# Performance work log

Measured on AMD Instinct MI355X. Metric: run time of the kernel, lower is better.

## Reference

```python
import jax, jax.numpy as jnp
import numpy as np

B, S, DIM = 4, 2048, 1024


def _xavier(key, shape):
    # xavier_uniform for a [out, in] Linear weight
    fan_in, fan_out = shape[1], shape[0]
    limit = float(np.sqrt(6.0 / (fan_in + fan_out)))
    return jax.random.uniform(key, shape, jnp.float32, -limit, limit)


def setup_inputs() -> dict:
    key = jax.random.key(0)
    ks = jax.random.split(key, 8)
    z_real = jax.random.normal(ks[0], (B, S, DIM), jnp.float32)
    z_imag = jax.random.normal(ks[1], (B, S, DIM), jnp.float32)
    wq_r = _xavier(ks[2], (DIM, DIM))
    wq_i = _xavier(ks[3], (DIM, DIM))
    wk_r = _xavier(ks[4], (DIM, DIM))
    wk_i = _xavier(ks[5], (DIM, DIM))
    wv_r = _xavier(ks[6], (DIM, DIM))
    wv_i = _xavier(ks[7], (DIM, DIM))
    # causal mask (0 = masked), broadcast over batch
    mask = jnp.tril(jnp.ones((S, S), jnp.int32))
    return {"z_real": z_real, "z_imag": z_imag,
            "wq_r": wq_r, "wq_i": wq_i,
            "wk_r": wk_r, "wk_i": wk_i,
            "wv_r": wv_r, "wv_i": wv_i,
            "mask": mask}


def _complex_linear(xr, xi, wr, wi):
    # torch Linear: y = x @ W^T
    yr = xr @ wr.T - xi @ wi.T
    yi = xi @ wr.T + xr @ wi.T
    return yr, yi


def reference(z_real, z_imag, wq_r, wq_i, wk_r, wk_i, wv_r, wv_i, mask):
    dim = z_real.shape[-1]
    scale = dim ** (-0.5)
    qr, qi = _complex_linear(z_real, z_imag, wq_r, wq_i)
    kr, ki = _complex_linear(z_real, z_imag, wk_r, wk_i)
    vr, vi = _complex_linear(z_real, z_imag, wv_r, wv_i)
    # cat([q.real, q.imag]) @ cat([k.real, k.imag])^T == qr@kr^T + qi@ki^T
    scores = (jnp.einsum('bsd,btd->bst', qr, kr)
              + jnp.einsum('bsd,btd->bst', qi, ki)) * scale  # [B,S,S]
    scores = jnp.where(mask == 0, -jnp.inf, scores)
    attn = jax.nn.softmax(scores, axis=-1)
    out_r = jnp.einsum('bst,btd->bsd', attn, vr)
    out_i = jnp.einsum('bst,btd->bsd', attn, vi)
    return jnp.stack([out_r, out_i], axis=0)  # [2,B,S,dim] = (real, imag)
```

## Files before the change

kernel.cpp:

```cpp
#include <hip/hip_runtime.h>
#include <hip/hip_bf16.h>
#include <hip/hip_fp16.h>

#define DIMK 1024
#define SEQ  2048
#define BATCH 4
#define NTOK (BATCH*SEQ)
#define PROJ_ELEMS ((size_t)NTOK*DIMK)
#define LD 2048

typedef unsigned short ushort_t;
typedef __attribute__((ext_vector_type(8))) short short8;
typedef __attribute__((ext_vector_type(4))) float float4v;

#define MFMA_BF16 __builtin_amdgcn_mfma_f32_16x16x32_bf16

__device__ __forceinline__ unsigned short f2bf(float f) {
    union { float f; unsigned int i; } x; x.f = f;
    unsigned int r = x.i + 0x7fffu + ((x.i >> 16) & 1u);
    return (unsigned short)(r >> 16);
}

__device__ __forceinline__ void gld_lds16(const void* g, void* l) {
    auto gp = reinterpret_cast<const __attribute__((address_space(1))) unsigned int*>(
        reinterpret_cast<uintptr_t>(g));
    auto lp = reinterpret_cast<__attribute__((address_space(3))) unsigned int*>(
        reinterpret_cast<uintptr_t>(l));
    __builtin_amdgcn_global_load_lds(gp, lp, 16, 0, 0);
}

__device__ __forceinline__ void stage2(const ushort_t* __restrict__ gbase,
                                       ushort_t* lbase, int kcol,
                                       int rg0, int g, int scol)
{
    gld_lds16(gbase + (size_t)(rg0 * 16 + g) * LD + kcol + scol,
              lbase + rg0 * 512);
    gld_lds16(gbase + (size_t)(rg0 * 16 + 16 + g) * LD + kcol + scol,
              lbase + rg0 * 512 + 512);
}

__device__ __forceinline__ void gemm_core256(
    const ushort_t* __restrict__ Arow,
    const ushort_t* __restrict__ Brow,
    int kend,
    ushort_t* Alds, ushort_t* Blds,
    float4v acc[8][4], int wid, int lane)
{
    const int g    = lane >> 2;
    const int sx   = lane & 3;
    const int scol = ((sx - (g >> 1)) & 3) * 8;
    const int r16  = lane & 15;
    const int quad = lane >> 4;
    const int roff = r16 * 32 + ((quad + (r16 >> 1)) & 3) * 8;
    const int wm8 = (wid >> 2) * 8;
    const int wn4 = (wid & 3) * 4;
    const int rg0 = wid * 2;
    const int NT = kend >> 6;

    short8 a0[4], b0[4], a1[4], b1[4];

    stage2(Brow, Blds,        0,  rg0, g, scol);
    stage2(Arow, Alds,        0,  rg0, g, scol);
    stage2(Brow, Blds + 8192, 32, rg0, g, scol);
    stage2(Arow, Alds + 8192, 32, rg0, g, scol);
    asm volatile("s_waitcnt vmcnt(4)" ::: "memory");
    __builtin_amdgcn_s_barrier();
    #pragma unroll
    for (int j = 0; j < 4; ++j)
        b0[j] = *(const short8*)(Blds + (wn4 + j) * 512 + roff);
    #pragma unroll
    for (int i = 0; i < 4; ++i)
        a0[i] = *(const short8*)(Alds + (wm8 + i) * 512 + roff);

    for (int t = 0; t < NT; ++t) {
        const int d     = (t & 1) << 14;
        const int dn    = d ^ 16384;
        const int knext = (t + 1) << 6;
        const bool pre  = (t + 1 < NT);

        #pragma unroll
        for (int j = 0; j < 4; ++j)
            b1[j] = *(const short8*)(Blds + d + (wn4 + j) * 512 + roff);
        #pragma unroll
        for (int i = 0; i < 4; ++i)
            a1[i] = *(const short8*)(Alds + d + (wm8 + 4 + i) * 512 + roff);
        if (pre) {
            stage2(Brow, Blds + dn, knext, rg0, g, scol);
            stage2(Arow, Alds + dn, knext, rg0, g, scol);
        }
        asm volatile("" ::: "memory");
        __builtin_amdgcn_s_barrier();
        __builtin_amdgcn_s_setprio(1);
        #pragma unroll
        for (int i = 0; i < 4; ++i)
            #pragma unroll
            for (int j = 0; j < 4; ++j)
                acc[i][j] = MFMA_BF16(a0[i], b0[j], acc[i][j], 0, 0, 0);
        __builtin_amdgcn_s_setprio(0);
        if (pre) asm volatile("s_waitcnt vmcnt(4)" ::: "memory");
        else     asm volatile("s_waitcnt vmcnt(0)" ::: "memory");
        __builtin_amdgcn_s_barrier();

        #pragma unroll
        for (int j = 0; j < 4; ++j)
            b0[j] = *(const short8*)(Blds + d + 8192 + (wn4 + j) * 512 + roff);
        #pragma unroll
        for (int i = 0; i < 4; ++i)
            a0[i] = *(const short8*)(Alds + d + 8192 + (wm8 + i) * 512 + roff);
        if (pre) {
            stage2(Brow, Blds + dn + 8192, knext + 32, rg0, g, scol);
            stage2(Arow, Alds + dn + 8192, knext + 32, rg0, g, scol);
        }
        asm volatile("" ::: "memory");
        __builtin_amdgcn_s_barrier();
        __builtin_amdgcn_s_setprio(1);
        #pragma unroll
        for (int i = 0; i < 4; ++i)
            #pragma unroll
            for (int j = 0; j < 4; ++j)
                acc[4 + i][j] = MFMA_BF16(a1[i], b1[j], acc[4 + i][j], 0, 0, 0);
        __builtin_amdgcn_s_setprio(0);
        asm volatile("" ::: "memory");
        __builtin_amdgcn_s_barrier();

        #pragma unroll
        for (int j = 0; j < 4; ++j)
            b1[j] = *(const short8*)(Blds + d + 8192 + (wn4 + j) * 512 + roff);
        #pragma unroll
        for (int i = 0; i < 4; ++i)
            a1[i] = *(const short8*)(Alds + d + 8192 + (wm8 + 4 + i) * 512 + roff);
        asm volatile("" ::: "memory");
        __builtin_amdgcn_s_barrier();
        __builtin_amdgcn_s_setprio(1);
        #pragma unroll
        for (int i = 0; i < 4; ++i)
            #pragma unroll
            for (int j = 0; j < 4; ++j)
                acc[i][j] = MFMA_BF16(a0[i], b0[j], acc[i][j], 0, 0, 0);
        __builtin_amdgcn_s_setprio(0);
        if (pre) asm volatile("s_waitcnt vmcnt(4)" ::: "memory");
        __builtin_amdgcn_s_barrier();

        if (pre) {
            #pragma unroll
            for (int j = 0; j < 4; ++j)
                b0[j] = *(const short8*)(Blds + dn + (wn4 + j) * 512 + roff);
            #pragma unroll
            for (int i = 0; i < 4; ++i)
                a0[i] = *(const short8*)(Alds + dn + (wm8 + i) * 512 + roff);
        }
        asm volatile("" ::: "memory");
        __builtin_amdgcn_s_barrier();
        __builtin_amdgcn_s_setprio(1);
        #pragma unroll
        for (int i = 0; i < 4; ++i)
            #pragma unroll
            for (int j = 0; j < 4; ++j)
                acc[4 + i][j] = MFMA_BF16(a1[i], b1[j], acc[4 + i][j], 0, 0, 0);
        __builtin_amdgcn_s_setprio(0);
        asm volatile("" ::: "memory");
        __builtin_amdgcn_s_barrier();
    }
}

__global__ __launch_bounds__(512, 2)
void gemm_proj(const ushort_t* __restrict__ A, const ushort_t* __restrict__ B,
               ushort_t* __restrict__ Cq, ushort_t* __restrict__ Ck,
               ushort_t* __restrict__ Cv)
{
    __shared__ ushort_t smem[65536];
    const int tid = threadIdx.x, wid = tid >> 6, lane = tid & 63;
    const int m0 = blockIdx.y * 256;
    const int n0g = blockIdx.x * 256;
    ushort_t* C = (n0g < 2048) ? Cq : ((n0g < 4096) ? Ck : Cv);
    const int n0 = n0g & 2047;
    float4v acc[8][4] = {};
    gemm_core256(A + (size_t)m0 * LD, B + (size_t)n0g * LD, 2048,
                 smem, smem + 32768, acc, wid, lane);

    const int wm = wid >> 2, wn = wid & 3;
    const int col16 = lane & 15, quad = lane >> 4;
    #pragma unroll
    for (int i = 0; i < 8; ++i)
        #pragma unroll
        for (int j = 0; j < 4; ++j) {
            const int n = n0 + wn * 64 + j * 16 + col16;
            #pragma unroll
            for (int r = 0; r < 4; ++r) {
                const int m = m0 + wm * 128 + i * 16 + quad * 4 + r;
                C[(size_t)m * LD + n] = f2bf(acc[i][j][r]);
            }
        }
}

__global__ __launch_bounds__(512, 2)
void gemm_scores(const ushort_t* __restrict__ Q, const ushort_t* __restrict__ K,
                 __half* __restrict__ S)
{
    const int jt = blockIdx.x, it = blockIdx.y, b = blockIdx.z;
    if (jt > it) return;
    __shared__ ushort_t smem[65536];
    const int tid = threadIdx.x, wid = tid >> 6, lane = tid & 63;
    const size_t boff = (size_t)b * SEQ * LD;
    float4v acc[8][4] = {};
    gemm_core256(Q + boff + (size_t)it * 256 * LD, K + boff + (size_t)jt * 256 * LD,
                 2048, smem, smem + 32768, acc, wid, lane);

    const int wm = wid >> 2, wn = wid & 3;
    const int col16 = lane & 15, quad = lane >> 4;
    const float scale = 0.03125f;
    __half* Sb = S + (size_t)b * SEQ * SEQ;
    #pragma unroll
    for (int i = 0; i < 8; ++i)
        #pragma unroll
        for (int j = 0; j < 4; ++j) {
            const int t = jt * 256 + wn * 64 + j * 16 + col16;
            #pragma unroll
            for (int r = 0; r < 4; ++r) {
                const int s = it * 256 + wm * 128 + i * 16 + quad * 4 + r;
                Sb[(size_t)s * SEQ + t] = __float2half(acc[i][j][r] * scale);
            }
        }
}

__global__ __launch_bounds__(512, 2)
void gemm_pv(const ushort_t* __restrict__ P, const ushort_t* __restrict__ VT,
             float* __restrict__ out)
{
    const int nt = blockIdx.x, mt = blockIdx.y, b = blockIdx.z;
    __shared__ ushort_t smem[65536];
    const int tid = threadIdx.x, wid = tid >> 6, lane = tid & 63;
    const int kend = (mt + 1) * 256;
    float4v acc[8][4] = {};
    gemm_core256(P + (size_t)b * SEQ * SEQ + (size_t)mt * 256 * LD,
                 VT + (size_t)b * LD * LD + (size_t)nt * 256 * LD,
                 kend, smem, smem + 32768, acc, wid, lane);

    const int wm = wid >> 2, wn = wid & 3;
    const int col16 = lane & 15, quad = lane >> 4;
    #pragma unroll
    for (int i = 0; i < 8; ++i)
        #pragma unroll
        for (int j = 0; j < 4; ++j) {
            const int n = nt * 256 + wn * 64 + j * 16 + col16;
            float* dst = out + ((n < 1024) ? 0 : PROJ_ELEMS);
            const int d = n & 1023;
            #pragma unroll
            for (int r = 0; r < 4; ++r) {
                const int s = mt * 256 + wm * 128 + i * 16 + quad * 4 + r;
                dst[((size_t)b * SEQ + s) * DIMK + d] = acc[i][j][r];
            }
        }
}

__global__ __launch_bounds__(256)
void zcat_kernel(const float* __restrict__ zr, const float* __restrict__ zi,
                 ushort_t* __restrict__ zcat)
{
    const size_t e = ((size_t)blockIdx.x * 256 + threadIdx.x) * 8;
    const size_t tok = e >> 11;
    const int c = (int)(e & 2047);
    const float* src = (c < 1024) ? (zr + tok * 1024 + c) : (zi + tok * 1024 + (c - 1024));
    float4 a = *(const float4*)src;
    float4 b = *(const float4*)(src + 4);
    ushort_t* d = zcat + e;
    d[0]=f2bf(a.x); d[1]=f2bf(a.y); d[2]=f2bf(a.z); d[3]=f2bf(a.w);
    d[4]=f2bf(b.x); d[5]=f2bf(b.y); d[6]=f2bf(b.z); d[7]=f2bf(b.w);
}

__global__ __launch_bounds__(256)
void wstack_kernel(const float* __restrict__ wr, const float* __restrict__ wi,
                   ushort_t* __restrict__ ws)
{
    const size_t e = ((size_t)blockIdx.x * 256 + threadIdx.x) * 8;
    const int n = (int)(e >> 11), c = (int)(e & 2047);
    const int n1 = n & 1023, c1 = c & 1023;
    const float* src;
    float sgn = 1.f;
    if (n < 1024) {
        if (c < 1024) src = wr + (size_t)n1 * 1024 + c1;
        else        { src = wi + (size_t)n1 * 1024 + c1; sgn = -1.f; }
    } else {
        src = ((c < 1024) ? wi : wr) + (size_t)n1 * 1024 + c1;
    }
    float4 a = *(const float4*)src;
    float4 b = *(const float4*)(src + 4);
    ushort_t* d = ws + e;
    d[0]=f2bf(sgn*a.x); d[1]=f2bf(sgn*a.y); d[2]=f2bf(sgn*a.z); d[3]=f2bf(sgn*a.w);
    d[4]=f2bf(sgn*b.x); d[5]=f2bf(sgn*b.y); d[6]=f2bf(sgn*b.z); d[7]=f2bf(sgn*b.w);
}

__global__ __launch_bounds__(256)
void transpose_v(const ushort_t* __restrict__ vcat, ushort_t* __restrict__ vt)
{
    __shared__ ushort_t tile[64][65];
    const int b = blockIdx.z;
    const int t0 = blockIdx.x * 64, c0 = blockIdx.y * 64;
    const int tid = threadIdx.x;
    const int r = tid >> 4, c4 = (tid & 15) * 4;
    const ushort_t* src = vcat + ((size_t)(b * SEQ + t0)) * LD + c0;
    #pragma unroll
    for (int p = 0; p < 4; ++p) {
        const int row = p * 16 + r;
        ushort4 v = *(const ushort4*)(src + (size_t)row * LD + c4);
        tile[row][c4+0]=v.x; tile[row][c4+1]=v.y; tile[row][c4+2]=v.z; tile[row][c4+3]=v.w;
    }
    __syncthreads();
    ushort_t* dst = vt + ((size_t)b * LD + c0) * LD + t0;
    #pragma unroll
    for (int p = 0; p < 4; ++p) {
        const int crow = p * 16 + r;
        ushort4 v;
        v.x = tile[c4+0][crow]; v.y = tile[c4+1][crow];
        v.z = tile[c4+2][crow]; v.w = tile[c4+3][crow];
        *(ushort4*)(dst + (size_t)crow * LD + c4) = v;
    }
}

__global__ __launch_bounds__(256)
void softmax_kernel(__half* __restrict__ sc)
{
    const int row = blockIdx.x;
    const int s = row & (SEQ - 1);
    __half* x = sc + (size_t)row * SEQ;
    ushort_t* xo = (ushort_t*)x;
    const int n = s + 1;
    const int tid = threadIdx.x, wave = tid >> 6, lane = tid & 63;
    __shared__ float redm[4], reds[4];

    float m = -1e30f;
    for (int i = tid; i < n; i += 256) m = fmaxf(m, __half2float(x[i]));
    #pragma unroll
    for (int off = 32; off > 0; off >>= 1) m = fmaxf(m, __shfl_down(m, off, 64));
    if (lane == 0) redm[wave] = m;
    __syncthreads();
    if (tid == 0) redm[0] = fmaxf(fmaxf(redm[0], redm[1]), fmaxf(redm[2], redm[3]));
    __syncthreads();
    m = redm[0];

    float l = 0.f;
    for (int i = tid; i < n; i += 256) l += __expf(__half2float(x[i]) - m);
    #pragma unroll
    for (int off = 32; off > 0; off >>= 1) l += __shfl_down(l, off, 64);
    if (lane == 0) reds[wave] = l;
    __syncthreads();
    if (tid == 0) reds[0] = reds[0] + reds[1] + reds[2] + reds[3];
    __syncthreads();
    const float inv = 1.0f / reds[0];

    const int npad = min(SEQ, ((s >> 8) + 1) << 8);
    for (int i = tid; i < npad; i += 256) {
        float v = (i < n) ? __expf(__half2float(x[i]) - m) * inv : 0.f;
        xo[i] = f2bf(v);
    }
}

extern "C" void kernel_launch(void* const* d_in, const int* in_sizes, int n_in,
                              void* d_out, int out_size, void* d_ws, size_t ws_size,
                              hipStream_t stream)
{
    const float* z_real = (const float*)d_in[0];
    const float* z_imag = (const float*)d_in[1];
    const float* wq_r   = (const float*)d_in[2];
    const float* wq_i   = (const float*)d_in[3];
    const float* wk_r   = (const float*)d_in[4];
    const float* wk_i   = (const float*)d_in[5];
    const float* wv_r   = (const float*)d_in[6];
    const float* wv_i   = (const float*)d_in[7];

    uint8_t* ws = (uint8_t*)d_ws;
    ushort_t* zcat = (ushort_t*)(ws + 0);
    ushort_t* wall = (ushort_t*)(ws + 33554432);
    ushort_t* wsq  = wall;
    ushort_t* wsk  = (ushort_t*)(ws + 33554432 + 8388608);
    ushort_t* wsv  = (ushort_t*)(ws + 33554432 + 16777216);
    ushort_t* qcat = (ushort_t*)(ws + 58720256);
    ushort_t* kcat = (ushort_t*)(ws + 92274688);
    ushort_t* vcat = (ushort_t*)(ws + 125829120);
    ushort_t* vt   = (ushort_t*)(ws + 0);
    __half*   sc   = (__half*)(ws + 125829120);
    float*    outp = (float*)d_out;

    zcat_kernel<<<dim3(8192), dim3(256), 0, stream>>>(z_real, z_imag, zcat);
    wstack_kernel<<<dim3(2048), dim3(256), 0, stream>>>(wq_r, wq_i, wsq);
    wstack_kernel<<<dim3(2048), dim3(256), 0, stream>>>(wk_r, wk_i, wsk);
    wstack_kernel<<<dim3(2048), dim3(256), 0, stream>>>(wv_r, wv_i, wsv);

    gemm_proj<<<dim3(24, 32), dim3(512), 0, stream>>>(zcat, wall, qcat, kcat, vcat);

    transpose_v<<<dim3(32, 32, 4), dim3(256), 0, stream>>>(vcat, vt);
    gemm_scores<<<dim3(8, 8, 4), dim3(512), 0, stream>>>(qcat, kcat, sc);
    softmax_kernel<<<dim3(NTOK), dim3(256), 0, stream>>>(sc);
    gemm_pv<<<dim3(8, 8, 4), dim3(512), 0, stream>>>((ushort_t*)sc, vt, outp);
}
```

Baseline: 518.9 us.

## Simplify GEMM main loop to two barrier phases per k-tile

Restructures the projection GEMM inner loop. Register double-buffering of A/B fragments across half-steps is dropped: each half-tile now loads all A and B fragments from LDS and issues all 32 MFMAs at once. This cuts the barriers per 64-wide k-tile from eight to two, to reduce synchronisation overhead. The cost is less overlap between LDS reads and MFMA inside a wave, so latency hiding now depends more on other resident waves.

Measured after the change: 473.0 us. 1.1x faster.

```diff
diff --git a/kernel.cpp b/kernel.cpp
--- a/kernel.cpp
+++ b/kernel.cpp
@@ -57,45 +57,44 @@
     const int rg0 = wid * 2;
     const int NT = kend >> 6;
 
-    short8 a0[4], b0[4], a1[4], b1[4];
-
     stage2(Brow, Blds,        0,  rg0, g, scol);
     stage2(Arow, Alds,        0,  rg0, g, scol);
     stage2(Brow, Blds + 8192, 32, rg0, g, scol);
     stage2(Arow, Alds + 8192, 32, rg0, g, scol);
     asm volatile("s_waitcnt vmcnt(4)" ::: "memory");
     __builtin_amdgcn_s_barrier();
-    #pragma unroll
-    for (int j = 0; j < 4; ++j)
-        b0[j] = *(const short8*)(Blds + (wn4 + j) * 512 + roff);
-    #pragma unroll
-    for (int i = 0; i < 4; ++i)
-        a0[i] = *(const short8*)(Alds + (wm8 + i) * 512 + roff);
 
     for (int t = 0; t < NT; ++t) {
         const int d     = (t & 1) << 14;
         const int dn    = d ^ 16384;
         const int knext = (t + 1) << 6;
         const bool pre  = (t + 1 < NT);
+        short8 af0[4], af1[4], bf[4];
 
         #pragma unroll
         for (int j = 0; j < 4; ++j)
-            b1[j] = *(const short8*)(Blds + d + (wn4 + j) * 512 + roff);
-        #pragma unroll
-        for (int i = 0; i < 4; ++i)
-            a1[i] = *(const short8*)(Alds + d + (wm8 + 4 + i) * 512 + roff);
+            bf[j] = *(const short8*)(Blds + d + (wn4 + j) * 512 + roff);
+        #pragma unroll
+        for (int i = 0; i < 4; ++i)
+            af0[i] = *(const short8*)(Alds + d + (wm8 + i) * 512 + roff);
+        #pragma unroll
+        for (int i = 0; i < 4; ++i)
+            af1[i] = *(const short8*)(Alds + d + (wm8 + 4 + i) * 512 + roff);
         if (pre) {
             stage2(Brow, Blds + dn, knext, rg0, g, scol);
             stage2(Arow, Alds + dn, knext, rg0, g, scol);
         }
-        asm volatile("" ::: "memory");
-        __builtin_amdgcn_s_barrier();
         __builtin_amdgcn_s_setprio(1);
         #pragma unroll
         for (int i = 0; i < 4; ++i)
             #pragma unroll
             for (int j = 0; j < 4; ++j)
-                acc[i][j] = MFMA_BF16(a0[i], b0[j], acc[i][j], 0, 0, 0);
+                acc[i][j] = MFMA_BF16(af0[i], bf[j], acc[i][j], 0, 0, 0);
+        #pragma unroll
+        for (int i = 0; i < 4; ++i)
+            #pragma unroll
+            for (int j = 0; j < 4; ++j)
+                acc[4 + i][j] = MFMA_BF16(af1[i], bf[j], acc[4 + i][j], 0, 0, 0);
         __builtin_amdgcn_s_setprio(0);
         if (pre) asm volatile("s_waitcnt vmcnt(4)" ::: "memory");
         else     asm volatile("s_waitcnt vmcnt(0)" ::: "memory");
@@ -103,62 +102,30 @@
 
         #pragma unroll
         for (int j = 0; j < 4; ++j)
-            b0[j] = *(const short8*)(Blds + d + 8192 + (wn4 + j) * 512 + roff);
-        #pragma unroll
-        for (int i = 0; i < 4; ++i)
-            a0[i] = *(const short8*)(Alds + d + 8192 + (wm8 + i) * 512 + roff);
+            bf[j] = *(const short8*)(Blds + d + 8192 + (wn4 + j) * 512 + roff);
+        #pragma unroll
+        for (int i = 0; i < 4; ++i)
+            af0[i] = *(const short8*)(Alds + d + 8192 + (wm8 + i) * 512 + roff);
+        #pragma unroll
+        for (int i = 0; i < 4; ++i)
+            af1[i] = *(const short8*)(Alds + d + 8192 + (wm8 + 4 + i) * 512 + roff);
         if (pre) {
             stage2(Brow, Blds + dn + 8192, knext + 32, rg0, g, scol);
             stage2(Arow, Alds + dn + 8192, knext + 32, rg0, g, scol);
         }
-        asm volatile("" ::: "memory");
-        __builtin_amdgcn_s_barrier();
         __builtin_amdgcn_s_setprio(1);
         #pragma unroll
         for (int i = 0; i < 4; ++i)
             #pragma unroll
             for (int j = 0; j < 4; ++j)
-                acc[4 + i][j] = MFMA_BF16(a1[i], b1[j], acc[4 + i][j], 0, 0, 0);
-        __builtin_amdgcn_s_setprio(0);
-        asm volatile("" ::: "memory");
-        __builtin_amdgcn_s_barrier();
-
-        #pragma unroll
-        for (int j = 0; j < 4; ++j)
-            b1[j] = *(const short8*)(Blds + d + 8192 + (wn4 + j) * 512 + roff);
-        #pragma unroll
-        for (int i = 0; i < 4; ++i)
-            a1[i] = *(const short8*)(Alds + d + 8192 + (wm8 + 4 + i) * 512 + roff);
-        asm volatile("" ::: "memory");
-        __builtin_amdgcn_s_barrier();
-        __builtin_amdgcn_s_setprio(1);
+                acc[i][j] = MFMA_BF16(af0[i], bf[j], acc[i][j], 0, 0, 0);
         #pragma unroll
         for (int i = 0; i < 4; ++i)
             #pragma unroll
             for (int j = 0; j < 4; ++j)
-                acc[i][j] = MFMA_BF16(a0[i], b0[j], acc[i][j], 0, 0, 0);
+                acc[4 + i][j] = MFMA_BF16(af1[i], bf[j], acc[4 + i][j], 0, 0, 0);
         __builtin_amdgcn_s_setprio(0);
         if (pre) asm volatile("s_waitcnt vmcnt(4)" ::: "memory");
-        __builtin_amdgcn_s_barrier();
-
-        if (pre) {
-            #pragma unroll
-            for (int j = 0; j < 4; ++j)
-                b0[j] = *(const short8*)(Blds + dn + (wn4 + j) * 512 + roff);
-            #pragma unroll
-            for (int i = 0; i < 4; ++i)
-                a0[i] = *(const short8*)(Alds + dn + (wm8 + i) * 512 + roff);
-        }
-        asm volatile("" ::: "memory");
-        __builtin_amdgcn_s_barrier();
-        __builtin_amdgcn_s_setprio(1);
-        #pragma unroll
-        for (int i = 0; i < 4; ++i)
-            #pragma unroll
-            for (int j = 0; j < 4; ++j)
-                acc[4 + i][j] = MFMA_BF16(a1[i], b1[j], acc[4 + i][j], 0, 0, 0);
-        __builtin_amdgcn_s_setprio(0);
-        asm volatile("" ::: "memory");
         __builtin_amdgcn_s_barrier();
     }
 }
```
